# Performance work log

Hardware: AMD Instinct MI355X
Metric: run time of the kernel (lower is better)

The kernel has to match this reference:

```python
import jax, jax.numpy as jnp
import numpy as np

N_NODES = 100000
N_EDGES = 3200000
D_IN = 256
D_OUT = 256


def setup_inputs() -> dict:
    key = jax.random.key(0)
    k1, k2, k3, k4, k5 = jax.random.split(key, 5)
    x = jax.random.normal(k1, (N_NODES, D_IN), dtype=jnp.float32)
    edge_val = jax.random.uniform(k2, (N_EDGES,), dtype=jnp.float32)
    weight = jax.random.normal(k3, (D_IN, D_OUT), dtype=jnp.float32)
    bias = jnp.zeros((D_OUT,), dtype=jnp.float32)
    edge_row = jax.random.randint(k4, (N_EDGES,), 0, N_NODES, dtype=jnp.int32)
    edge_col = jax.random.randint(k5, (N_EDGES,), 0, N_NODES, dtype=jnp.int32)
    return {"x": x, "edge_val": edge_val, "weight": weight, "bias": bias,
            "edge_row": edge_row, "edge_col": edge_col}


def reference(x, edge_val, weight, bias, edge_row, edge_col):
    # Dense feature transform: support = x @ W  -> [N, D_OUT]
    support = x @ weight
    # SpMM with COO adjacency: out[i] = sum_{e: row[e]=i} val[e] * support[col[e]]
    messages = edge_val[:, None] * support[edge_col]        # [E, D_OUT] gather
    out = jax.ops.segment_sum(messages, edge_row, num_segments=N_NODES)
    return out + bias
```

## Files before the change

### kernel.cpp

```cpp
#include <hip/hip_runtime.h>

#define D 256
#define BSHIFT 7
#define BROWS 128
#define CHUNK 8192

typedef __attribute__((ext_vector_type(8))) short bf16x8;
typedef __attribute__((ext_vector_type(4))) float f32x4;

__device__ inline ushort f2bf_rne(float f) {
    uint u = __builtin_bit_cast(uint, f);
    return (ushort)((u + 0x7FFFu + ((u >> 16) & 1u)) >> 16);
}

__global__ __launch_bounds__(256) void conv_wt(const float* __restrict__ w,
                                               ushort* __restrict__ wt) {
    const int idx = blockIdx.x * 256 + threadIdx.x;
    const int n = idx >> 8, k = idx & 255;
    wt[n * 256 + k] = f2bf_rne(w[k * 256 + n]);
}

__global__ __launch_bounds__(256) void gemm_mfma(const float* __restrict__ x,
                                                 const ushort* __restrict__ wt,
                                                 ushort* __restrict__ sup,
                                                 int N) {
    __shared__ ushort As[64 * 256];
    const int tid = threadIdx.x;
    const int wv  = tid >> 6;
    const int ln  = tid & 63;
    const int row0 = blockIdx.x * 64;

    for (int i = tid; i < 64 * 64; i += 256) {
        const int r = i >> 6, c = i & 63;
        int gr = row0 + r;
        if (gr >= N) gr = N - 1;
        const float4 xv = *(const float4*)(x + (size_t)gr * D + c * 4);
        ushort4 b;
        b.x = f2bf_rne(xv.x); b.y = f2bf_rne(xv.y);
        b.z = f2bf_rne(xv.z); b.w = f2bf_rne(xv.w);
        const int byte = (r * 512 + c * 8) ^ ((r & 7) << 4);
        *(ushort4*)((char*)As + byte) = b;
    }
    __syncthreads();

    f32x4 acc[16];
#pragma unroll
    for (int n = 0; n < 16; ++n) acc[n] = (f32x4){0.f, 0.f, 0.f, 0.f};

    const int arow = wv * 16 + (ln & 15);
    const int ksub = (ln >> 4) * 16;
    const ushort* wbase = wt + (ln & 15) * 256;

#pragma unroll
    for (int kk = 0; kk < 8; ++kk) {
        const int abyte = (arow * 512 + kk * 64 + ksub) ^ ((arow & 7) << 4);
        const bf16x8 af = *(const bf16x8*)((const char*)As + abyte);
        const ushort* wp = wbase + kk * 32 + (ln >> 4) * 8;
#pragma unroll
        for (int n = 0; n < 16; ++n) {
            const bf16x8 bf = *(const bf16x8*)(wp + n * 16 * 256);
            acc[n] = __builtin_amdgcn_mfma_f32_16x16x32_bf16(af, bf, acc[n], 0, 0, 0);
        }
    }

    const int crow = row0 + wv * 16 + (ln >> 4) * 4;
    const int ccol = ln & 15;
#pragma unroll
    for (int n = 0; n < 16; ++n) {
#pragma unroll
        for (int reg = 0; reg < 4; ++reg) {
            const int r = crow + reg;
            if (r < N) sup[(size_t)r * D + n * 16 + ccol] = f2bf_rne(acc[n][reg]);
        }
    }
}

__global__ __launch_bounds__(256) void zero_ints(int* __restrict__ p, int n) {
    const int i = blockIdx.x * 256 + threadIdx.x;
    if (i < n) p[i] = 0;
}

__global__ __launch_bounds__(256) void bucket_hist(const int* __restrict__ edge_row,
                                                   int* __restrict__ bcnt,
                                                   int E, int NB) {
    __shared__ int bh[1024];
    const int tid = threadIdx.x;
    for (int i = tid; i < 1024; i += 256) bh[i] = 0;
    __syncthreads();

    const int e0 = blockIdx.x * CHUNK;
    const int e1 = min(e0 + CHUNK, E);
    for (int i = e0 + tid * 4; i < e1; i += 1024) {
        if (i + 3 < e1) {
            const int4 r = *(const int4*)(edge_row + i);
            atomicAdd(&bh[r.x >> BSHIFT], 1);
            atomicAdd(&bh[r.y >> BSHIFT], 1);
            atomicAdd(&bh[r.z >> BSHIFT], 1);
            atomicAdd(&bh[r.w >> BSHIFT], 1);
        } else {
            for (int j = i; j < e1; ++j) atomicAdd(&bh[edge_row[j] >> BSHIFT], 1);
        }
    }
    __syncthreads();

    for (int b = tid; b < NB; b += 256) {
        const int c = bh[b];
        if (c) atomicAdd(&bcnt[b], c);
    }
}

__global__ __launch_bounds__(512) void bucket_scan(const int* __restrict__ bcnt,
                                                   int* __restrict__ bstart,
                                                   int* __restrict__ bcursor,
                                                   int* __restrict__ row_start,
                                                   int NB, int N, int E) {
    __shared__ int psum[512];
    const int tid = threadIdx.x;
    int v[4];
    int s = 0;
#pragma unroll
    for (int k = 0; k < 4; ++k) {
        const int i = tid * 4 + k;
        v[k] = (i < NB) ? bcnt[i] : 0;
        s += v[k];
    }
    psum[tid] = s;
    __syncthreads();
#pragma unroll
    for (int off = 1; off < 512; off <<= 1) {
        const int t = (tid >= off) ? psum[tid - off] : 0;
        __syncthreads();
        psum[tid] += t;
        __syncthreads();
    }
    int run = psum[tid] - s;
#pragma unroll
    for (int k = 0; k < 4; ++k) {
        const int i = tid * 4 + k;
        if (i < NB) { bstart[i] = run; bcursor[i] = run; }
        run += v[k];
    }
    if (tid == 0) { bstart[NB] = E; row_start[N] = E; }
}

__global__ __launch_bounds__(256) void bucket_scatter(
        const int* __restrict__ edge_row, const int* __restrict__ edge_col,
        const float* __restrict__ edge_val, int* __restrict__ bucket_cursor,
        unsigned long long* __restrict__ ebuck, int E, int NB) {
    __shared__ int cur[1024];
    const int tid = threadIdx.x;
    const int e0  = blockIdx.x * CHUNK;
    const int e1  = min(e0 + CHUNK, E);

    for (int i = tid; i < 1024; i += 256) cur[i] = 0;
    __syncthreads();

    for (int e = e0 + tid; e < e1; e += 256)
        atomicAdd(&cur[edge_row[e] >> BSHIFT], 1);
    __syncthreads();

    for (int b = tid; b < NB; b += 256) {
        const int c = cur[b];
        cur[b] = (c > 0) ? atomicAdd(&bucket_cursor[b], c) : 0;
    }
    __syncthreads();

    for (int e = e0 + tid; e < e1; e += 256) {
        const int r = edge_row[e];
        const int b = r >> BSHIFT;
        const int pos = atomicAdd(&cur[b], 1);
        const unsigned long long pk =
            ((unsigned long long)(uint)f2bf_rne(edge_val[e]) << 48) |
            ((unsigned long long)(uint)edge_col[e] << 17) | (uint)r;
        ebuck[pos] = pk;
    }
}

__device__ inline long long pack_cv(int c, float v) {
    return (long long)(((unsigned long long)__builtin_bit_cast(uint, v) << 32) |
                       (uint)c);
}

__global__ __launch_bounds__(256) void fine_scatter(
        const unsigned long long* __restrict__ ebuck,
        const int* __restrict__ bstart,
        long long* __restrict__ epair,
        int* __restrict__ row_start, int N) {
    __shared__ int cnt[BROWS];
    __shared__ int cur[BROWS];
    const int tid = threadIdx.x;
    const int r0  = blockIdx.x << BSHIFT;
    const int s   = bstart[blockIdx.x];
    const int e   = bstart[blockIdx.x + 1];

    if (tid < BROWS) cnt[tid] = 0;
    __syncthreads();

    for (int i = s + tid; i < e; i += 256)
        atomicAdd(&cnt[(int)(ebuck[i] & 0x1FFFFu) - r0], 1);
    __syncthreads();

    if (tid < BROWS) cur[tid] = cnt[tid];
    __syncthreads();
#pragma unroll
    for (int off = 1; off < BROWS; off <<= 1) {
        const int t = (tid < BROWS && tid >= off) ? cur[tid - off] : 0;
        __syncthreads();
        if (tid < BROWS) cur[tid] += t;
        __syncthreads();
    }
    if (tid < BROWS) {
        const int rs = s + cur[tid] - cnt[tid];
        cur[tid] = rs;
        const int row = r0 + tid;
        if (row < N) row_start[row] = rs;
    }
    __syncthreads();

    for (int i = s + tid; i < e; i += 256) {
        const unsigned long long pk = ebuck[i];
        const int  r  = (int)(pk & 0x1FFFFu) - r0;
        const int  c  = (int)((pk >> 17) & 0x1FFFFu);
        const float v = __builtin_bit_cast(float, (uint)(pk >> 48) << 16);
        const int pos = atomicAdd(&cur[r], 1);
        epair[pos] = pack_cv(c, v);
    }
}

__global__ __launch_bounds__(256) void accumulate(const ushort* __restrict__ sup,
                                                  const int* __restrict__ row_start,
                                                  const long long* __restrict__ epair,
                                                  const float* __restrict__ bias,
                                                  float* __restrict__ out, int N) {
    const int row = blockIdx.x * 4 + (threadIdx.x >> 6);
    if (row >= N) return;
    const int lane = threadIdx.x & 63;
    const int lofs = lane * 4;

    const int s = row_start[row];
    const int e = row_start[row + 1];

    f32x4 a[8];
    a[0] = *(const f32x4*)(bias + lofs);
#pragma unroll
    for (int q = 1; q < 8; ++q) a[q] = (f32x4){0.f, 0.f, 0.f, 0.f};

    for (int base = s; base < e; base += 64) {
        const int idx = base + lane;
        long long pk = 0;
        if (idx < e) pk = __builtin_nontemporal_load(epair + idx);
        const int   c = (int)(uint)pk;
        const float v = __builtin_bit_cast(float, (uint)((unsigned long long)pk >> 32));
        const int n = min(64, e - base);
        int j = 0;
        for (; j + 7 < n; j += 8) {
            int   cq[8];
            float vq[8];
            uint2 uq[8];
#pragma unroll
            for (int q = 0; q < 8; ++q) {
                cq[q] = __shfl(c, j + q);
                vq[q] = __shfl(v, j + q);
            }
#pragma unroll
            for (int q = 0; q < 8; ++q)
                uq[q] = *(const uint2*)(sup + ((uint)cq[q] << 8) + lofs);
#pragma unroll
            for (int q = 0; q < 8; ++q) {
                const float f0 = __builtin_bit_cast(float, uq[q].x << 16);
                const float f1 = __builtin_bit_cast(float, uq[q].x & 0xFFFF0000u);
                const float f2 = __builtin_bit_cast(float, uq[q].y << 16);
                const float f3 = __builtin_bit_cast(float, uq[q].y & 0xFFFF0000u);
                a[q][0] = fmaf(vq[q], f0, a[q][0]);
                a[q][1] = fmaf(vq[q], f1, a[q][1]);
                a[q][2] = fmaf(vq[q], f2, a[q][2]);
                a[q][3] = fmaf(vq[q], f3, a[q][3]);
            }
        }
        for (; j < n; ++j) {
            const int   c0 = __shfl(c, j);
            const float v0 = __shfl(v, j);
            const uint2 u  = *(const uint2*)(sup + ((uint)c0 << 8) + lofs);
            const float f0 = __builtin_bit_cast(float, u.x << 16);
            const float f1 = __builtin_bit_cast(float, u.x & 0xFFFF0000u);
            const float f2 = __builtin_bit_cast(float, u.y << 16);
            const float f3 = __builtin_bit_cast(float, u.y & 0xFFFF0000u);
            a[0][0] = fmaf(v0, f0, a[0][0]);
            a[0][1] = fmaf(v0, f1, a[0][1]);
            a[0][2] = fmaf(v0, f2, a[0][2]);
            a[0][3] = fmaf(v0, f3, a[0][3]);
        }
    }
#pragma unroll
    for (int q = 1; q < 8; ++q) {
        a[0][0] += a[q][0]; a[0][1] += a[q][1];
        a[0][2] += a[q][2]; a[0][3] += a[q][3];
    }
    __builtin_nontemporal_store(a[0], (f32x4*)(out + (size_t)row * D + lofs));
}

extern "C" void kernel_launch(void* const* d_in, const int* in_sizes, int n_in,
                              void* d_out, int out_size, void* d_ws, size_t ws_size,
                              hipStream_t stream) {
    const float* x        = (const float*)d_in[0];
    const float* edge_val = (const float*)d_in[1];
    const float* weight   = (const float*)d_in[2];
    const float* bias     = (const float*)d_in[3];
    const int*   edge_row = (const int*)d_in[4];
    const int*   edge_col = (const int*)d_in[5];
    float*       out      = (float*)d_out;

    const int N = in_sizes[0] / D;
    const int E = in_sizes[1];

    char* ws = (char*)d_ws;
    size_t off = 0;
    auto carve = [&](size_t bytes) -> char* {
        char* p = ws + off;
        off = (off + bytes + 255) & ~(size_t)255;
        return p;
    };

    const int NB = (N + BROWS - 1) / BROWS;

    ushort* sup = (ushort*)carve((size_t)N * D * sizeof(ushort));
    ushort* wt  = (ushort*)carve((size_t)D * D * sizeof(ushort));
    unsigned long long* ebuck =
        (unsigned long long*)carve((size_t)E * sizeof(unsigned long long));
    long long* epair = (long long*)carve((size_t)E * sizeof(long long));
    int* row_start = (int*)carve((size_t)(N + 1) * sizeof(int));
    int* bcnt      = (int*)carve((size_t)NB * sizeof(int));
    int* bstart    = (int*)carve((size_t)(NB + 1) * sizeof(int));
    int* bcursor   = (int*)carve((size_t)NB * sizeof(int));

    const int nchunk = (E + CHUNK - 1) / CHUNK;

    conv_wt<<<(D * D) / 256, 256, 0, stream>>>(weight, wt);
    gemm_mfma<<<(N + 63) / 64, 256, 0, stream>>>(x, wt, sup, N);

    zero_ints<<<(NB + 255) / 256, 256, 0, stream>>>(bcnt, NB);
    bucket_hist<<<nchunk, 256, 0, stream>>>(edge_row, bcnt, E, NB);
    bucket_scan<<<1, 512, 0, stream>>>(bcnt, bstart, bcursor, row_start, NB, N, E);

    bucket_scatter<<<nchunk, 256, 0, stream>>>(edge_row, edge_col, edge_val,
                                               bcursor, ebuck, E, NB);
    fine_scatter<<<NB, 256, 0, stream>>>(ebuck, bstart, epair, row_start, N);

    accumulate<<<(N + 3) / 4, 256, 0, stream>>>(sup, row_start, epair, bias, out, N);
}
```

Measured before the change: 448.1 us.

## Fuse GEMM with bucket scatter and fine sort into accumulate via LDS

Merges the weight conversion with the bucket-count zeroing, and runs the MFMA GEMM blocks and the edge bucket-scatter blocks in one heterogeneous launch so the two independent phases overlap. The fine per-row sort now happens in LDS inside the accumulate kernel, so the epair and row_start global buffers and their round trip through memory are gone. The trade-off is 128-row blocks with 4 waves each instead of one wave per row, which lowers parallelism for the gather phase and adds a 48KB LDS footprint that limits occupancy. A slow fallback path handles buckets larger than the LDS capacity.

```diff
diff --git a/kernel.cpp b/kernel.cpp
--- a/kernel.cpp
+++ b/kernel.cpp
@@ -4,6 +4,7 @@
 #define BSHIFT 7
 #define BROWS 128
 #define CHUNK 8192
+#define CAP 6144
 
 typedef __attribute__((ext_vector_type(8))) short bf16x8;
 typedef __attribute__((ext_vector_type(4))) float f32x4;
@@ -13,71 +14,16 @@
     return (ushort)((u + 0x7FFFu + ((u >> 16) & 1u)) >> 16);
 }
 
-__global__ __launch_bounds__(256) void conv_wt(const float* __restrict__ w,
-                                               ushort* __restrict__ wt) {
+__global__ __launch_bounds__(256) void prep(const float* __restrict__ w,
+                                            ushort* __restrict__ wt,
+                                            int* __restrict__ bcnt, int NB) {
     const int idx = blockIdx.x * 256 + threadIdx.x;
-    const int n = idx >> 8, k = idx & 255;
-    wt[n * 256 + k] = f2bf_rne(w[k * 256 + n]);
-}
-
-__global__ __launch_bounds__(256) void gemm_mfma(const float* __restrict__ x,
-                                                 const ushort* __restrict__ wt,
-                                                 ushort* __restrict__ sup,
-                                                 int N) {
-    __shared__ ushort As[64 * 256];
-    const int tid = threadIdx.x;
-    const int wv  = tid >> 6;
-    const int ln  = tid & 63;
-    const int row0 = blockIdx.x * 64;
-
-    for (int i = tid; i < 64 * 64; i += 256) {
-        const int r = i >> 6, c = i & 63;
-        int gr = row0 + r;
-        if (gr >= N) gr = N - 1;
-        const float4 xv = *(const float4*)(x + (size_t)gr * D + c * 4);
-        ushort4 b;
-        b.x = f2bf_rne(xv.x); b.y = f2bf_rne(xv.y);
-        b.z = f2bf_rne(xv.z); b.w = f2bf_rne(xv.w);
-        const int byte = (r * 512 + c * 8) ^ ((r & 7) << 4);
-        *(ushort4*)((char*)As + byte) = b;
-    }
-    __syncthreads();
-
-    f32x4 acc[16];
-#pragma unroll
-    for (int n = 0; n < 16; ++n) acc[n] = (f32x4){0.f, 0.f, 0.f, 0.f};
-
-    const int arow = wv * 16 + (ln & 15);
-    const int ksub = (ln >> 4) * 16;
-    const ushort* wbase = wt + (ln & 15) * 256;
-
-#pragma unroll
-    for (int kk = 0; kk < 8; ++kk) {
-        const int abyte = (arow * 512 + kk * 64 + ksub) ^ ((arow & 7) << 4);
-        const bf16x8 af = *(const bf16x8*)((const char*)As + abyte);
-        const ushort* wp = wbase + kk * 32 + (ln >> 4) * 8;
-#pragma unroll
-        for (int n = 0; n < 16; ++n) {
-            const bf16x8 bf = *(const bf16x8*)(wp + n * 16 * 256);
-            acc[n] = __builtin_amdgcn_mfma_f32_16x16x32_bf16(af, bf, acc[n], 0, 0, 0);
-        }
-    }
-
-    const int crow = row0 + wv * 16 + (ln >> 4) * 4;
-    const int ccol = ln & 15;
-#pragma unroll
-    for (int n = 0; n < 16; ++n) {
-#pragma unroll
-        for (int reg = 0; reg < 4; ++reg) {
-            const int r = crow + reg;
-            if (r < N) sup[(size_t)r * D + n * 16 + ccol] = f2bf_rne(acc[n][reg]);
-        }
-    }
-}
-
-__global__ __launch_bounds__(256) void zero_ints(int* __restrict__ p, int n) {
-    const int i = blockIdx.x * 256 + threadIdx.x;
-    if (i < n) p[i] = 0;
+    if (idx < D * D) {
+        const int n = idx >> 8, k = idx & 255;
+        wt[n * 256 + k] = f2bf_rne(w[k * 256 + n]);
+    } else if (idx - D * D < NB) {
+        bcnt[idx - D * D] = 0;
+    }
 }
 
 __global__ __launch_bounds__(256) void bucket_hist(const int* __restrict__ edge_row,
@@ -112,8 +58,7 @@
 __global__ __launch_bounds__(512) void bucket_scan(const int* __restrict__ bcnt,
                                                    int* __restrict__ bstart,
                                                    int* __restrict__ bcursor,
-                                                   int* __restrict__ row_start,
-                                                   int NB, int N, int E) {
+                                                   int NB, int E) {
     __shared__ int psum[512];
     const int tid = threadIdx.x;
     int v[4];
@@ -140,163 +85,228 @@
         if (i < NB) { bstart[i] = run; bcursor[i] = run; }
         run += v[k];
     }
-    if (tid == 0) { bstart[NB] = E; row_start[N] = E; }
-}
-
-__global__ __launch_bounds__(256) void bucket_scatter(
+    if (tid == 0) bstart[NB] = E;
+}
+
+union SMemGS {
+    ushort As[64 * 256];
+    int    cur[1024];
+};
+
+__global__ __launch_bounds__(256) void gemm_scatter(
+        const float* __restrict__ x, const ushort* __restrict__ wt,
+        ushort* __restrict__ sup, int N, int ngemm,
         const int* __restrict__ edge_row, const int* __restrict__ edge_col,
-        const float* __restrict__ edge_val, int* __restrict__ bucket_cursor,
+        const float* __restrict__ edge_val, int* __restrict__ bcursor,
         unsigned long long* __restrict__ ebuck, int E, int NB) {
-    __shared__ int cur[1024];
+    __shared__ SMemGS sm;
     const int tid = threadIdx.x;
-    const int e0  = blockIdx.x * CHUNK;
-    const int e1  = min(e0 + CHUNK, E);
-
-    for (int i = tid; i < 1024; i += 256) cur[i] = 0;
-    __syncthreads();
-
-    for (int e = e0 + tid; e < e1; e += 256)
-        atomicAdd(&cur[edge_row[e] >> BSHIFT], 1);
-    __syncthreads();
-
-    for (int b = tid; b < NB; b += 256) {
-        const int c = cur[b];
-        cur[b] = (c > 0) ? atomicAdd(&bucket_cursor[b], c) : 0;
-    }
-    __syncthreads();
-
-    for (int e = e0 + tid; e < e1; e += 256) {
-        const int r = edge_row[e];
-        const int b = r >> BSHIFT;
-        const int pos = atomicAdd(&cur[b], 1);
-        const unsigned long long pk =
-            ((unsigned long long)(uint)f2bf_rne(edge_val[e]) << 48) |
-            ((unsigned long long)(uint)edge_col[e] << 17) | (uint)r;
-        ebuck[pos] = pk;
-    }
-}
-
-__device__ inline long long pack_cv(int c, float v) {
-    return (long long)(((unsigned long long)__builtin_bit_cast(uint, v) << 32) |
-                       (uint)c);
-}
-
-__global__ __launch_bounds__(256) void fine_scatter(
+
+    if (blockIdx.x < ngemm) {
+        const int wv  = tid >> 6;
+        const int ln  = tid & 63;
+        const int row0 = blockIdx.x * 64;
+
+        for (int i = tid; i < 64 * 64; i += 256) {
+            const int r = i >> 6, c = i & 63;
+            int gr = row0 + r;
+            if (gr >= N) gr = N - 1;
+            const float4 xv = *(const float4*)(x + (size_t)gr * D + c * 4);
+            ushort4 b;
+            b.x = f2bf_rne(xv.x); b.y = f2bf_rne(xv.y);
+            b.z = f2bf_rne(xv.z); b.w = f2bf_rne(xv.w);
+            const int byte = (r * 512 + c * 8) ^ ((r & 7) << 4);
+            *(ushort4*)((char*)sm.As + byte) = b;
+        }
+        __syncthreads();
+
+        f32x4 acc[16];
+#pragma unroll
+        for (int n = 0; n < 16; ++n) acc[n] = (f32x4){0.f, 0.f, 0.f, 0.f};
+
+        const int arow = wv * 16 + (ln & 15);
+        const int ksub = (ln >> 4) * 16;
+        const ushort* wbase = wt + (ln & 15) * 256;
+
+#pragma unroll
+        for (int kk = 0; kk < 8; ++kk) {
+            const int abyte = (arow * 512 + kk * 64 + ksub) ^ ((arow & 7) << 4);
+            const bf16x8 af = *(const bf16x8*)((const char*)sm.As + abyte);
+            const ushort* wp = wbase + kk * 32 + (ln >> 4) * 8;
+#pragma unroll
+            for (int n = 0; n < 16; ++n) {
+                const bf16x8 bf = *(const bf16x8*)(wp + n * 16 * 256);
+                acc[n] = __builtin_amdgcn_mfma_f32_16x16x32_bf16(af, bf, acc[n], 0, 0, 0);
+            }
+        }
+
+        const int crow = row0 + wv * 16 + (ln >> 4) * 4;
+        const int ccol = ln & 15;
+#pragma unroll
+        for (int n = 0; n < 16; ++n) {
+#pragma unroll
+            for (int reg = 0; reg < 4; ++reg) {
+                const int r = crow + reg;
+                if (r < N) sup[(size_t)r * D + n * 16 + ccol] = f2bf_rne(acc[n][reg]);
+            }
+        }
+    } else {
+        const int e0 = (blockIdx.x - ngemm) * CHUNK;
+        const int e1 = min(e0 + CHUNK, E);
+
+        for (int i = tid; i < 1024; i += 256) sm.cur[i] = 0;
+        __syncthreads();
+
+        for (int e = e0 + tid; e < e1; e += 256)
+            atomicAdd(&sm.cur[edge_row[e] >> BSHIFT], 1);
+        __syncthreads();
+
+        for (int b = tid; b < NB; b += 256) {
+            const int c = sm.cur[b];
+            sm.cur[b] = (c > 0) ? atomicAdd(&bcursor[b], c) : 0;
+        }
+        __syncthreads();
+
+        for (int e = e0 + tid; e < e1; e += 256) {
+            const int r = edge_row[e];
+            const int b = r >> BSHIFT;
+            const int pos = atomicAdd(&sm.cur[b], 1);
+            const unsigned long long pk =
+                ((unsigned long long)(uint)f2bf_rne(edge_val[e]) << 48) |
+                ((unsigned long long)(uint)edge_col[e] << 17) | (uint)r;
+            ebuck[pos] = pk;
+        }
+    }
+}
+
+__global__ __launch_bounds__(256) void fine_accumulate(
+        const ushort* __restrict__ sup,
         const unsigned long long* __restrict__ ebuck,
         const int* __restrict__ bstart,
-        long long* __restrict__ epair,
-        int* __restrict__ row_start, int N) {
+        const float* __restrict__ bias,
+        float* __restrict__ out, int N) {
+    __shared__ unsigned long long ed[CAP];
     __shared__ int cnt[BROWS];
     __shared__ int cur[BROWS];
-    const int tid = threadIdx.x;
-    const int r0  = blockIdx.x << BSHIFT;
-    const int s   = bstart[blockIdx.x];
-    const int e   = bstart[blockIdx.x + 1];
-
-    if (tid < BROWS) cnt[tid] = 0;
-    __syncthreads();
-
-    for (int i = s + tid; i < e; i += 256)
-        atomicAdd(&cnt[(int)(ebuck[i] & 0x1FFFFu) - r0], 1);
-    __syncthreads();
-
-    if (tid < BROWS) cur[tid] = cnt[tid];
-    __syncthreads();
-#pragma unroll
-    for (int off = 1; off < BROWS; off <<= 1) {
-        const int t = (tid < BROWS && tid >= off) ? cur[tid - off] : 0;
-        __syncthreads();
-        if (tid < BROWS) cur[tid] += t;
-        __syncthreads();
-    }
-    if (tid < BROWS) {
-        const int rs = s + cur[tid] - cnt[tid];
-        cur[tid] = rs;
-        const int row = r0 + tid;
-        if (row < N) row_start[row] = rs;
-    }
-    __syncthreads();
-
-    for (int i = s + tid; i < e; i += 256) {
-        const unsigned long long pk = ebuck[i];
-        const int  r  = (int)(pk & 0x1FFFFu) - r0;
-        const int  c  = (int)((pk >> 17) & 0x1FFFFu);
-        const float v = __builtin_bit_cast(float, (uint)(pk >> 48) << 16);
-        const int pos = atomicAdd(&cur[r], 1);
-        epair[pos] = pack_cv(c, v);
-    }
-}
-
-__global__ __launch_bounds__(256) void accumulate(const ushort* __restrict__ sup,
-                                                  const int* __restrict__ row_start,
-                                                  const long long* __restrict__ epair,
-                                                  const float* __restrict__ bias,
-                                                  float* __restrict__ out, int N) {
-    const int row = blockIdx.x * 4 + (threadIdx.x >> 6);
-    if (row >= N) return;
-    const int lane = threadIdx.x & 63;
+    __shared__ int srow[BROWS + 1];
+    const int tid  = threadIdx.x;
+    const int lane = tid & 63;
+    const int wv   = tid >> 6;
+    const int r0   = blockIdx.x << BSHIFT;
+    const int s    = bstart[blockIdx.x];
+    const int e    = bstart[blockIdx.x + 1];
+    const int m    = e - s;
     const int lofs = lane * 4;
-
-    const int s = row_start[row];
-    const int e = row_start[row + 1];
-
-    f32x4 a[8];
-    a[0] = *(const f32x4*)(bias + lofs);
-#pragma unroll
-    for (int q = 1; q < 8; ++q) a[q] = (f32x4){0.f, 0.f, 0.f, 0.f};
-
-    for (int base = s; base < e; base += 64) {
-        const int idx = base + lane;
-        long long pk = 0;
-        if (idx < e) pk = __builtin_nontemporal_load(epair + idx);
-        const int   c = (int)(uint)pk;
-        const float v = __builtin_bit_cast(float, (uint)((unsigned long long)pk >> 32));
-        const int n = min(64, e - base);
-        int j = 0;
-        for (; j + 7 < n; j += 8) {
-            int   cq[8];
-            float vq[8];
-            uint2 uq[8];
-#pragma unroll
-            for (int q = 0; q < 8; ++q) {
-                cq[q] = __shfl(c, j + q);
-                vq[q] = __shfl(v, j + q);
-            }
-#pragma unroll
-            for (int q = 0; q < 8; ++q)
-                uq[q] = *(const uint2*)(sup + ((uint)cq[q] << 8) + lofs);
-#pragma unroll
-            for (int q = 0; q < 8; ++q) {
-                const float f0 = __builtin_bit_cast(float, uq[q].x << 16);
-                const float f1 = __builtin_bit_cast(float, uq[q].x & 0xFFFF0000u);
-                const float f2 = __builtin_bit_cast(float, uq[q].y << 16);
-                const float f3 = __builtin_bit_cast(float, uq[q].y & 0xFFFF0000u);
-                a[q][0] = fmaf(vq[q], f0, a[q][0]);
-                a[q][1] = fmaf(vq[q], f1, a[q][1]);
-                a[q][2] = fmaf(vq[q], f2, a[q][2]);
-                a[q][3] = fmaf(vq[q], f3, a[q][3]);
-            }
-        }
-        for (; j < n; ++j) {
-            const int   c0 = __shfl(c, j);
-            const float v0 = __shfl(v, j);
-            const uint2 u  = *(const uint2*)(sup + ((uint)c0 << 8) + lofs);
-            const float f0 = __builtin_bit_cast(float, u.x << 16);
-            const float f1 = __builtin_bit_cast(float, u.x & 0xFFFF0000u);
-            const float f2 = __builtin_bit_cast(float, u.y << 16);
-            const float f3 = __builtin_bit_cast(float, u.y & 0xFFFF0000u);
-            a[0][0] = fmaf(v0, f0, a[0][0]);
-            a[0][1] = fmaf(v0, f1, a[0][1]);
-            a[0][2] = fmaf(v0, f2, a[0][2]);
-            a[0][3] = fmaf(v0, f3, a[0][3]);
-        }
-    }
-#pragma unroll
-    for (int q = 1; q < 8; ++q) {
-        a[0][0] += a[q][0]; a[0][1] += a[q][1];
-        a[0][2] += a[q][2]; a[0][3] += a[q][3];
-    }
-    __builtin_nontemporal_store(a[0], (f32x4*)(out + (size_t)row * D + lofs));
+    const f32x4 bias_v = *(const f32x4*)(bias + lofs);
+
+    if (m <= CAP) {
+        if (tid < BROWS) cnt[tid] = 0;
+        __syncthreads();
+
+        for (int i = tid; i < m; i += 256)
+            atomicAdd(&cnt[(int)(ebuck[s + i] & 0x1FFFFu) - r0], 1);
+        __syncthreads();
+
+        if (tid < BROWS) cur[tid] = cnt[tid];
+        __syncthreads();
+#pragma unroll
+        for (int off = 1; off < BROWS; off <<= 1) {
+            const int t = (tid < BROWS && tid >= off) ? cur[tid - off] : 0;
+            __syncthreads();
+            if (tid < BROWS) cur[tid] += t;
+            __syncthreads();
+        }
+        if (tid < BROWS) {
+            const int ex = cur[tid] - cnt[tid];
+            srow[tid] = ex;
+            cur[tid]  = ex;
+        }
+        if (tid == 0) srow[BROWS] = m;
+        __syncthreads();
+
+        for (int i = tid; i < m; i += 256) {
+            const unsigned long long pk = ebuck[s + i];
+            const int r = (int)(pk & 0x1FFFFu) - r0;
+            const int pos = atomicAdd(&cur[r], 1);
+            ed[pos] = pk;
+        }
+        __syncthreads();
+
+        for (int r = wv; r < BROWS; r += 4) {
+            const int row = r0 + r;
+            if (row >= N) break;
+            const int rs = srow[r], re = srow[r + 1];
+
+            f32x4 a[8];
+            a[0] = bias_v;
+#pragma unroll
+            for (int q = 1; q < 8; ++q) a[q] = (f32x4){0.f, 0.f, 0.f, 0.f};
+
+            int j = rs;
+            for (; j + 7 < re; j += 8) {
+                int cq[8]; float vq[8]; uint2 uq[8];
+#pragma unroll
+                for (int q = 0; q < 8; ++q) {
+                    const unsigned long long pk = ed[j + q];
+                    cq[q] = (int)((pk >> 17) & 0x1FFFFu);
+                    vq[q] = __builtin_bit_cast(float, (uint)(pk >> 48) << 16);
+                }
+#pragma unroll
+                for (int q = 0; q < 8; ++q)
+                    uq[q] = *(const uint2*)(sup + ((uint)cq[q] << 8) + lofs);
+#pragma unroll
+                for (int q = 0; q < 8; ++q) {
+                    const float f0 = __builtin_bit_cast(float, uq[q].x << 16);
+                    const float f1 = __builtin_bit_cast(float, uq[q].x & 0xFFFF0000u);
+                    const float f2 = __builtin_bit_cast(float, uq[q].y << 16);
+                    const float f3 = __builtin_bit_cast(float, uq[q].y & 0xFFFF0000u);
+                    a[q][0] = fmaf(vq[q], f0, a[q][0]);
+                    a[q][1] = fmaf(vq[q], f1, a[q][1]);
+                    a[q][2] = fmaf(vq[q], f2, a[q][2]);
+                    a[q][3] = fmaf(vq[q], f3, a[q][3]);
+                }
+            }
+            for (; j < re; ++j) {
+                const unsigned long long pk = ed[j];
+                const int   c0 = (int)((pk >> 17) & 0x1FFFFu);
+                const float v0 = __builtin_bit_cast(float, (uint)(pk >> 48) << 16);
+                const uint2 u  = *(const uint2*)(sup + ((uint)c0 << 8) + lofs);
+                const float f0 = __builtin_bit_cast(float, u.x << 16);
+                const float f1 = __builtin_bit_cast(float, u.x & 0xFFFF0000u);
+                const float f2 = __builtin_bit_cast(float, u.y << 16);
+                const float f3 = __builtin_bit_cast(float, u.y & 0xFFFF0000u);
+                a[0][0] = fmaf(v0, f0, a[0][0]);
+                a[0][1] = fmaf(v0, f1, a[0][1]);
+                a[0][2] = fmaf(v0, f2, a[0][2]);
+                a[0][3] = fmaf(v0, f3, a[0][3]);
+            }
+#pragma unroll
+            for (int q = 1; q < 8; ++q) {
+                a[0][0] += a[q][0]; a[0][1] += a[q][1];
+                a[0][2] += a[q][2]; a[0][3] += a[q][3];
+            }
+            __builtin_nontemporal_store(a[0], (f32x4*)(out + (size_t)row * D + lofs));
+        }
+    } else {
+        for (int r = wv; r < BROWS; r += 4) {
+            const int row = r0 + r;
+            if (row >= N) break;
+            f32x4 a = bias_v;
+            for (int i = s; i < e; ++i) {
+                const unsigned long long pk = ebuck[i];
+                if ((int)(pk & 0x1FFFFu) - r0 == r) {
+                    const int   c0 = (int)((pk >> 17) & 0x1FFFFu);
+                    const float v0 = __builtin_bit_cast(float, (uint)(pk >> 48) << 16);
+                    const uint2 u  = *(const uint2*)(sup + ((uint)c0 << 8) + lofs);
+                    a[0] = fmaf(v0, __builtin_bit_cast(float, u.x << 16), a[0]);
+                    a[1] = fmaf(v0, __builtin_bit_cast(float, u.x & 0xFFFF0000u), a[1]);
+                    a[2] = fmaf(v0, __builtin_bit_cast(float, u.y << 16), a[2]);
+                    a[3] = fmaf(v0, __builtin_bit_cast(float, u.y & 0xFFFF0000u), a[3]);
+                }
+            }
+            __builtin_nontemporal_store(a, (f32x4*)(out + (size_t)row * D + lofs));
+        }
+    }
 }
 
 extern "C" void kernel_launch(void* const* d_in, const int* in_sizes, int n_in,
@@ -327,24 +337,20 @@
     ushort* wt  = (ushort*)carve((size_t)D * D * sizeof(ushort));
     unsigned long long* ebuck =
         (unsigned long long*)carve((size_t)E * sizeof(unsigned long long));
-    long long* epair = (long long*)carve((size_t)E * sizeof(long long));
-    int* row_start = (int*)carve((size_t)(N + 1) * sizeof(int));
-    int* bcnt      = (int*)carve((size_t)NB * sizeof(int));
-    int* bstart    = (int*)carve((size_t)(NB + 1) * sizeof(int));
-    int* bcursor   = (int*)carve((size_t)NB * sizeof(int));
-
+    int* bcnt    = (int*)carve((size_t)NB * sizeof(int));
+    int* bstart  = (int*)carve((size_t)(NB + 1) * sizeof(int));
+    int* bcursor = (int*)carve((size_t)NB * sizeof(int));
+
+    const int ngemm  = (N + 63) / 64;
     const int nchunk = (E + CHUNK - 1) / CHUNK;
 
-    conv_wt<<<(D * D) / 256, 256, 0, stream>>>(weight, wt);
-    gemm_mfma<<<(N + 63) / 64, 256, 0, stream>>>(x, wt, sup, N);
-
-    zero_ints<<<(NB + 255) / 256, 256, 0, stream>>>(bcnt, NB);
+    prep<<<(D * D + NB + 255) / 256, 256, 0, stream>>>(weight, wt, bcnt, NB);
+
     bucket_hist<<<nchunk, 256, 0, stream>>>(edge_row, bcnt, E, NB);
-    bucket_scan<<<1, 512, 0, stream>>>(bcnt, bstart, bcursor, row_start, NB, N, E);
-
-    bucket_scatter<<<nchunk, 256, 0, stream>>>(edge_row, edge_col, edge_val,
-                                               bcursor, ebuck, E, NB);
-    fine_scatter<<<NB, 256, 0, stream>>>(ebuck, bstart, epair, row_start, N);
-
-    accumulate<<<(N + 3) / 4, 256, 0, stream>>>(sup, row_start, epair, bias, out, N);
-}
+    bucket_scan<<<1, 512, 0, stream>>>(bcnt, bstart, bcursor, NB, E);
+
+    gemm_scatter<<<ngemm + nchunk, 256, 0, stream>>>(
+        x, wt, sup, N, ngemm, edge_row, edge_col, edge_val, bcursor, ebuck, E, NB);
+
+    fine_accumulate<<<NB, 256, 0, stream>>>(sup, ebuck, bstart, bias, out, N);
+}
```

After: 478.9 us. 6.9% more time.

## Merge GEMM and bucket scatter into one heterogeneous launch; fuse prep kernels

Applied to the files above, without the earlier changes.

Merges the weight conversion and histogram zeroing into one prep kernel. Folds the dense GEMM and the coarse bucket scatter into a single launch, where the first blocks do GEMM tiles and the rest do edge scatter chunks, with shared memory overlaid in a union. This removes launches and lets the compute-bound GEMM overlap with the memory and atomic-bound scatter. In exchange, the union sizes shared memory to the GEMM's 32KB for scatter blocks as well, which may limit their occupancy.

```diff
diff --git a/kernel.cpp b/kernel.cpp
--- a/kernel.cpp
+++ b/kernel.cpp
@@ -13,71 +13,16 @@
     return (ushort)((u + 0x7FFFu + ((u >> 16) & 1u)) >> 16);
 }
 
-__global__ __launch_bounds__(256) void conv_wt(const float* __restrict__ w,
-                                               ushort* __restrict__ wt) {
+__global__ __launch_bounds__(256) void prep(const float* __restrict__ w,
+                                            ushort* __restrict__ wt,
+                                            int* __restrict__ bcnt, int NB) {
     const int idx = blockIdx.x * 256 + threadIdx.x;
-    const int n = idx >> 8, k = idx & 255;
-    wt[n * 256 + k] = f2bf_rne(w[k * 256 + n]);
-}
-
-__global__ __launch_bounds__(256) void gemm_mfma(const float* __restrict__ x,
-                                                 const ushort* __restrict__ wt,
-                                                 ushort* __restrict__ sup,
-                                                 int N) {
-    __shared__ ushort As[64 * 256];
-    const int tid = threadIdx.x;
-    const int wv  = tid >> 6;
-    const int ln  = tid & 63;
-    const int row0 = blockIdx.x * 64;
-
-    for (int i = tid; i < 64 * 64; i += 256) {
-        const int r = i >> 6, c = i & 63;
-        int gr = row0 + r;
-        if (gr >= N) gr = N - 1;
-        const float4 xv = *(const float4*)(x + (size_t)gr * D + c * 4);
-        ushort4 b;
-        b.x = f2bf_rne(xv.x); b.y = f2bf_rne(xv.y);
-        b.z = f2bf_rne(xv.z); b.w = f2bf_rne(xv.w);
-        const int byte = (r * 512 + c * 8) ^ ((r & 7) << 4);
-        *(ushort4*)((char*)As + byte) = b;
-    }
-    __syncthreads();
-
-    f32x4 acc[16];
-#pragma unroll
-    for (int n = 0; n < 16; ++n) acc[n] = (f32x4){0.f, 0.f, 0.f, 0.f};
-
-    const int arow = wv * 16 + (ln & 15);
-    const int ksub = (ln >> 4) * 16;
-    const ushort* wbase = wt + (ln & 15) * 256;
-
-#pragma unroll
-    for (int kk = 0; kk < 8; ++kk) {
-        const int abyte = (arow * 512 + kk * 64 + ksub) ^ ((arow & 7) << 4);
-        const bf16x8 af = *(const bf16x8*)((const char*)As + abyte);
-        const ushort* wp = wbase + kk * 32 + (ln >> 4) * 8;
-#pragma unroll
-        for (int n = 0; n < 16; ++n) {
-            const bf16x8 bf = *(const bf16x8*)(wp + n * 16 * 256);
-            acc[n] = __builtin_amdgcn_mfma_f32_16x16x32_bf16(af, bf, acc[n], 0, 0, 0);
-        }
-    }
-
-    const int crow = row0 + wv * 16 + (ln >> 4) * 4;
-    const int ccol = ln & 15;
-#pragma unroll
-    for (int n = 0; n < 16; ++n) {
-#pragma unroll
-        for (int reg = 0; reg < 4; ++reg) {
-            const int r = crow + reg;
-            if (r < N) sup[(size_t)r * D + n * 16 + ccol] = f2bf_rne(acc[n][reg]);
-        }
-    }
-}
-
-__global__ __launch_bounds__(256) void zero_ints(int* __restrict__ p, int n) {
-    const int i = blockIdx.x * 256 + threadIdx.x;
-    if (i < n) p[i] = 0;
+    if (idx < D * D) {
+        const int n = idx >> 8, k = idx & 255;
+        wt[n * 256 + k] = f2bf_rne(w[k * 256 + n]);
+    } else if (idx - D * D < NB) {
+        bcnt[idx - D * D] = 0;
+    }
 }
 
 __global__ __launch_bounds__(256) void bucket_hist(const int* __restrict__ edge_row,
@@ -143,36 +88,94 @@
     if (tid == 0) { bstart[NB] = E; row_start[N] = E; }
 }
 
-__global__ __launch_bounds__(256) void bucket_scatter(
+union SMemGS {
+    ushort As[64 * 256];
+    int    cur[1024];
+};
+
+__global__ __launch_bounds__(256) void gemm_scatter(
+        const float* __restrict__ x, const ushort* __restrict__ wt,
+        ushort* __restrict__ sup, int N, int ngemm,
         const int* __restrict__ edge_row, const int* __restrict__ edge_col,
-        const float* __restrict__ edge_val, int* __restrict__ bucket_cursor,
+        const float* __restrict__ edge_val, int* __restrict__ bcursor,
         unsigned long long* __restrict__ ebuck, int E, int NB) {
-    __shared__ int cur[1024];
+    __shared__ SMemGS sm;
     const int tid = threadIdx.x;
-    const int e0  = blockIdx.x * CHUNK;
-    const int e1  = min(e0 + CHUNK, E);
-
-    for (int i = tid; i < 1024; i += 256) cur[i] = 0;
-    __syncthreads();
-
-    for (int e = e0 + tid; e < e1; e += 256)
-        atomicAdd(&cur[edge_row[e] >> BSHIFT], 1);
-    __syncthreads();
-
-    for (int b = tid; b < NB; b += 256) {
-        const int c = cur[b];
-        cur[b] = (c > 0) ? atomicAdd(&bucket_cursor[b], c) : 0;
-    }
-    __syncthreads();
-
-    for (int e = e0 + tid; e < e1; e += 256) {
-        const int r = edge_row[e];
-        const int b = r >> BSHIFT;
-        const int pos = atomicAdd(&cur[b], 1);
-        const unsigned long long pk =
-            ((unsigned long long)(uint)f2bf_rne(edge_val[e]) << 48) |
-            ((unsigned long long)(uint)edge_col[e] << 17) | (uint)r;
-        ebuck[pos] = pk;
+
+    if (blockIdx.x < ngemm) {
+        const int wv  = tid >> 6;
+        const int ln  = tid & 63;
+        const int row0 = blockIdx.x * 64;
+
+        for (int i = tid; i < 64 * 64; i += 256) {
+            const int r = i >> 6, c = i & 63;
+            int gr = row0 + r;
+            if (gr >= N) gr = N - 1;
+            const float4 xv = *(const float4*)(x + (size_t)gr * D + c * 4);
+            ushort4 b;
+            b.x = f2bf_rne(xv.x); b.y = f2bf_rne(xv.y);
+            b.z = f2bf_rne(xv.z); b.w = f2bf_rne(xv.w);
+            const int byte = (r * 512 + c * 8) ^ ((r & 7) << 4);
+            *(ushort4*)((char*)sm.As + byte) = b;
+        }
+        __syncthreads();
+
+        f32x4 acc[16];
+#pragma unroll
+        for (int n = 0; n < 16; ++n) acc[n] = (f32x4){0.f, 0.f, 0.f, 0.f};
+
+        const int arow = wv * 16 + (ln & 15);
+        const int ksub = (ln >> 4) * 16;
+        const ushort* wbase = wt + (ln & 15) * 256;
+
+#pragma unroll
+        for (int kk = 0; kk < 8; ++kk) {
+            const int abyte = (arow * 512 + kk * 64 + ksub) ^ ((arow & 7) << 4);
+            const bf16x8 af = *(const bf16x8*)((const char*)sm.As + abyte);
+            const ushort* wp = wbase + kk * 32 + (ln >> 4) * 8;
+#pragma unroll
+            for (int n = 0; n < 16; ++n) {
+                const bf16x8 bf = *(const bf16x8*)(wp + n * 16 * 256);
+                acc[n] = __builtin_amdgcn_mfma_f32_16x16x32_bf16(af, bf, acc[n], 0, 0, 0);
+            }
+        }
+
+        const int crow = row0 + wv * 16 + (ln >> 4) * 4;
+        const int ccol = ln & 15;
+#pragma unroll
+        for (int n = 0; n < 16; ++n) {
+#pragma unroll
+            for (int reg = 0; reg < 4; ++reg) {
+                const int r = crow + reg;
+                if (r < N) sup[(size_t)r * D + n * 16 + ccol] = f2bf_rne(acc[n][reg]);
+            }
+        }
+    } else {
+        const int e0 = (blockIdx.x - ngemm) * CHUNK;
+        const int e1 = min(e0 + CHUNK, E);
+
+        for (int i = tid; i < 1024; i += 256) sm.cur[i] = 0;
+        __syncthreads();
+
+        for (int e = e0 + tid; e < e1; e += 256)
+            atomicAdd(&sm.cur[edge_row[e] >> BSHIFT], 1);
+        __syncthreads();
+
+        for (int b = tid; b < NB; b += 256) {
+            const int c = sm.cur[b];
+            sm.cur[b] = (c > 0) ? atomicAdd(&bcursor[b], c) : 0;
+        }
+        __syncthreads();
+
+        for (int e = e0 + tid; e < e1; e += 256) {
+            const int r = edge_row[e];
+            const int b = r >> BSHIFT;
+            const int pos = atomicAdd(&sm.cur[b], 1);
+            const unsigned long long pk =
+                ((unsigned long long)(uint)f2bf_rne(edge_val[e]) << 48) |
+                ((unsigned long long)(uint)edge_col[e] << 17) | (uint)r;
+            ebuck[pos] = pk;
+        }
     }
 }
 
@@ -333,17 +336,17 @@
     int* bstart    = (int*)carve((size_t)(NB + 1) * sizeof(int));
     int* bcursor   = (int*)carve((size_t)NB * sizeof(int));
 
+    const int ngemm  = (N + 63) / 64;
     const int nchunk = (E + CHUNK - 1) / CHUNK;
 
-    conv_wt<<<(D * D) / 256, 256, 0, stream>>>(weight, wt);
-    gemm_mfma<<<(N + 63) / 64, 256, 0, stream>>>(x, wt, sup, N);
-
-    zero_ints<<<(NB + 255) / 256, 256, 0, stream>>>(bcnt, NB);
+    prep<<<(D * D + NB + 255) / 256, 256, 0, stream>>>(weight, wt, bcnt, NB);
+
     bucket_hist<<<nchunk, 256, 0, stream>>>(edge_row, bcnt, E, NB);
     bucket_scan<<<1, 512, 0, stream>>>(bcnt, bstart, bcursor, row_start, NB, N, E);
 
-    bucket_scatter<<<nchunk, 256, 0, stream>>>(edge_row, edge_col, edge_val,
-                                               bcursor, ebuck, E, NB);
+    gemm_scatter<<<ngemm + nchunk, 256, 0, stream>>>(
+        x, wt, sup, N, ngemm, edge_row, edge_col, edge_val, bcursor, ebuck, E, NB);
+
     fine_scatter<<<NB, 256, 0, stream>>>(ebuck, bstart, epair, row_start, N);
 
     accumulate<<<(N + 3) / 4, 256, 0, stream>>>(sup, row_start, epair, bias, out, N);
```

Measured after the change: 409.5 us. 8.6% less time.
